# Kernel tuning notes

Measured on AMD Instinct MI355X. Metric: run time of the kernel, lower is better.

Reference implementation:

```python
import jax, jax.numpy as jnp
import numpy as np

HIDDEN = 128
N_RBF = 20
K = 16
CUTOFF = 5.0


def setup_inputs() -> dict:
    key = jax.random.key(0)
    ks = jax.random.split(key, 12)
    B, N, D = 8, 4096, HIDDEN
    edge_in = 2 * D + N_RBF  # 276
    s = 0.02
    return {
        "h": jax.random.normal(ks[0], (B, N, D), jnp.float32),
        "positions": jax.random.normal(ks[1], (B, N, 3), jnp.float32),
        # edge MLP: Linear(276->128), SiLU, Linear(128->128), SiLU
        "ew1": jax.random.normal(ks[2], (edge_in, D), jnp.float32) * s,
        "eb1": jnp.zeros((D,), jnp.float32),
        "ew2": jax.random.normal(ks[3], (D, D), jnp.float32) * s,
        "eb2": jnp.zeros((D,), jnp.float32),
        # node MLP: Linear(256->128), SiLU, (Dropout=identity in eval), Linear(128->128)
        "nw1": jax.random.normal(ks[4], (2 * D, D), jnp.float32) * s,
        "nb1": jnp.zeros((D,), jnp.float32),
        "nw2": jax.random.normal(ks[5], (D, D), jnp.float32) * s,
        "nb2": jnp.zeros((D,), jnp.float32),
        # LayerNorm
        "gamma": jnp.ones((D,), jnp.float32),
        "beta": jnp.zeros((D,), jnp.float32),
    }


def reference(h, positions, ew1, eb1, ew2, eb2, nw1, nb1, nw2, nb2, gamma, beta):
    B, N, D = h.shape
    k = min(K, N - 1)

    # ---- kNN graph build (dense pairwise, self masked with +inf) ----
    diff = positions[:, :, None, :] - positions[:, None, :, :]      # [B,N,N,3]
    dists = jnp.sqrt(jnp.sum(diff * diff, axis=-1) + 1e-8)          # [B,N,N]
    eye = jnp.eye(N, dtype=bool)
    dists_masked = jnp.where(eye[None], jnp.inf, dists)
    _, edge_idx = jax.lax.top_k(-dists_masked, k)                   # [B,N,k] smallest dists
    edge_dist = jnp.take_along_axis(dists_masked, edge_idx, axis=-1)  # [B,N,k]
    edge_mask = edge_dist < CUTOFF                                  # [B,N,k]

    # ---- RBF distance encoding (non-trainable buffers) ----
    centers = jnp.linspace(0.0, CUTOFF, N_RBF)                      # [n_rbf]
    widths = (CUTOFF / N_RBF) ** (-2)
    rbf = jnp.exp(-widths * (edge_dist[..., None] - centers) ** 2)  # [B,N,k,n_rbf]

    # ---- gather neighbor features ----
    h_j = jax.vmap(lambda hb, ib: hb[ib])(h, edge_idx)              # [B,N,k,D]
    h_i = jnp.broadcast_to(h[:, :, None, :], h_j.shape)             # [B,N,k,D]
    edge_features = jnp.concatenate([h_i, h_j, rbf], axis=-1)       # [B,N,k,2D+n_rbf]

    # ---- edge MLP + mask + scatter-sum aggregate ----
    m = jax.nn.silu(edge_features @ ew1 + eb1)
    m = jax.nn.silu(m @ ew2 + eb2)
    m = m * edge_mask[..., None].astype(m.dtype)
    agg = jnp.sum(m, axis=2)                                        # [B,N,D]

    # ---- node MLP (dropout is identity at eval) + residual + LayerNorm ----
    node_in = jnp.concatenate([h, agg], axis=-1)                    # [B,N,2D]
    update = jax.nn.silu(node_in @ nw1 + nb1) @ nw2 + nb2
    x = h + update
    mu = jnp.mean(x, axis=-1, keepdims=True)
    var = jnp.mean((x - mu) ** 2, axis=-1, keepdims=True)
    return (x - mu) / jnp.sqrt(var + 1e-5) * gamma + beta
```

## Files before the change

kernel.cpp:

```cpp
#include <hip/hip_runtime.h>
#include <hip/hip_bf16.h>

#define HID 128
#define NRBF 20
#define KNN 16
#define NNODE 4096
#define NBATCH 8

typedef __attribute__((ext_vector_type(8))) short short8;
typedef __attribute__((ext_vector_type(4))) float f32x4;

__device__ __forceinline__ short f2bf(float x) {
  __hip_bfloat16 b = __float2bfloat16(x);
  return __builtin_bit_cast(short, b);
}
__device__ __forceinline__ float silu_f(float x) {
  return x * __builtin_amdgcn_rcpf(1.0f + __expf(-x));
}
__device__ __forceinline__ short8 cv8(const float* p) {
  f32x4 a = *(const f32x4*)p;
  f32x4 b = *(const f32x4*)(p + 4);
  short8 r;
  r[0]=f2bf(a[0]); r[1]=f2bf(a[1]); r[2]=f2bf(a[2]); r[3]=f2bf(a[3]);
  r[4]=f2bf(b[0]); r[5]=f2bf(b[1]); r[6]=f2bf(b[2]); r[7]=f2bf(b[3]);
  return r;
}

__global__ __launch_bounds__(512)
void knn_kernel(const float* __restrict__ pos,
                int* __restrict__ eidx, float* __restrict__ edist)
{
  __shared__ f32x4 posL4[NNODE];
  __shared__ float d2b[8][128];
  __shared__ int   jb[8][128];
  __shared__ int   cntL[8];

  const int tid  = threadIdx.x;
  const int wv   = tid >> 6;
  const int lane = tid & 63;
  const int b    = blockIdx.x >> 7;
  const int grp  = blockIdx.x & 127;

  const float* pb = pos + (size_t)b * NNODE * 3;
  for (int idx = tid; idx < NNODE; idx += 512) {
    f32x4 v; v[0] = pb[idx*3]; v[1] = pb[idx*3+1]; v[2] = pb[idx*3+2]; v[3] = 0.f;
    posL4[idx] = v;
  }
  __syncthreads();

  const int i0 = grp * 32 + wv * 4;
  f32x4 pn[4];
  #pragma unroll
  for (int n = 0; n < 4; ++n) pn[n] = posL4[i0 + n];

  float vmin[4] = {3.0e38f, 3.0e38f, 3.0e38f, 3.0e38f};
  for (int t = 0; t < 64; ++t) {
    const int j = t * 64 + lane;
    f32x4 p = posL4[j];
    #pragma unroll
    for (int n = 0; n < 4; ++n) {
      float dx = __fsub_rn(pn[n][0], p[0]);
      float dy = __fsub_rn(pn[n][1], p[1]);
      float dz = __fsub_rn(pn[n][2], p[2]);
      float d2 = __fadd_rn(__fadd_rn(__fmul_rn(dx,dx), __fmul_rn(dy,dy)), __fmul_rn(dz,dz));
      if (j == i0 + n) d2 = 3.0e38f;
      vmin[n] = fminf(vmin[n], d2);
    }
  }

  float Ts[4];
  #pragma unroll
  for (int n = 0; n < 4; ++n) {
    float v = vmin[n];
    #pragma unroll
    for (int k = 2; k <= 64; k <<= 1) {
      #pragma unroll
      for (int jj = k >> 1; jj > 0; jj >>= 1) {
        float o = __shfl_xor(v, jj);
        const bool up   = ((lane & k) == 0);
        const bool lowl = ((lane & jj) == 0);
        float mn = fminf(v, o), mx = fmaxf(v, o);
        v = (up == lowl) ? mn : mx;
      }
    }
    Ts[n] = __shfl(v, 15);
  }

  #pragma unroll 1
  for (int n = 0; n < 4; ++n) {
    const int i = i0 + n;
    const float pix = pn[n][0], piy = pn[n][1], piz = pn[n][2];
    const float T = Ts[n];

    if (lane == 0) cntL[wv] = 0;
    for (int t = 0; t < 64; ++t) {
      const int j = t * 64 + lane;
      f32x4 p = posL4[j];
      float dx = __fsub_rn(pix, p[0]);
      float dy = __fsub_rn(piy, p[1]);
      float dz = __fsub_rn(piz, p[2]);
      float d2 = __fadd_rn(__fadd_rn(__fmul_rn(dx,dx), __fmul_rn(dy,dy)), __fmul_rn(dz,dz));
      bool ok = (j != i) && (d2 <= T);
      if (ok) {
        int p2 = atomicAdd(&cntL[wv], 1);
        if (p2 < 128) { d2b[wv][p2] = d2; jb[wv][p2] = j; }
      }
    }
    int cnt = cntL[wv];
    if (cnt > 128) cnt = 128;

    for (int s = lane; s < cnt; s += 64) {
      float dm = d2b[wv][s]; int jm = jb[wv][s];
      int rank = 0;
      for (int c = 0; c < cnt; ++c) {
        float dc = d2b[wv][c]; int jc = jb[wv][c];
        if (dc < dm || (dc == dm && jc < jm)) ++rank;
      }
      if (rank < KNN) {
        size_t base = ((size_t)b * NNODE + i) * KNN;
        eidx[base + rank]  = b * NNODE + jm;
        edist[base + rank] = sqrtf(__fadd_rn(dm, 1e-8f));
      }
    }
  }
}

#define ENPW 16

__global__ __launch_bounds__(512)
void edge_kernel(const float* __restrict__ h,
                 const int* __restrict__ eidx, const float* __restrict__ edist,
                 const float* __restrict__ ew1, const float* __restrict__ eb1,
                 const float* __restrict__ ew2, const float* __restrict__ eb2,
                 float* __restrict__ agg)
{
  __shared__ __attribute__((aligned(16))) short8 F1[9*8*64];
  __shared__ __attribute__((aligned(16))) short8 F2[4*8*64];
  __shared__ __attribute__((aligned(16))) short m1s[8][2048];

  const int tid = threadIdx.x;
  for (int f = tid; f < 9*8*64; f += 512) {
    int kc = f >> 9, rem = f & 511, nf = rem >> 6, ln = rem & 63;
    int kb = kc*32 + (ln >> 4)*8, col = nf*16 + (ln & 15);
    short8 v;
    #pragma unroll
    for (int e = 0; e < 8; ++e) {
      int k = kb + e;
      v[e] = (k < 276) ? f2bf(ew1[k*128 + col]) : (short)0;
    }
    F1[f] = v;
  }
  for (int f = tid; f < 4*8*64; f += 512) {
    int kc = f >> 9, rem = f & 511, nf = rem >> 6, ln = rem & 63;
    int kb = kc*32 + (ln >> 4)*8, col = nf*16 + (ln & 15);
    short8 v;
    #pragma unroll
    for (int e = 0; e < 8; ++e) v[e] = f2bf(ew2[(kb + e)*128 + col]);
    F2[f] = v;
  }
  __syncthreads();

  const int wv = tid >> 6, lane = tid & 63;
  const int lo = lane & 15, hi = lane >> 4;
  short* m1w = &m1s[wv][0];

  float b1v[8], b2v[8];
  #pragma unroll
  for (int nf = 0; nf < 8; ++nf) {
    b1v[nf] = eb1[nf*16 + lo];
    b2v[nf] = eb2[nf*16 + lo];
  }
  int wbase[4], xmask[4], rbase[4];
  #pragma unroll
  for (int q = 0; q < 4; ++q) {
    int row = hi*4 + q;
    wbase[q] = (row << 8) + (lo << 1);
    xmask[q] = (row & 7) << 4;
  }
  #pragma unroll
  for (int kc = 0; kc < 4; ++kc)
    rbase[kc] = ((lo << 8) + ((kc*32 + hi*8) << 1)) ^ ((lo & 7) << 4);

  const f32x4 zero4 = {0.f, 0.f, 0.f, 0.f};
  const int nbase = (blockIdx.x * 8 + wv) * ENPW;

  #pragma unroll 1
  for (int it = 0; it < ENPW/2; ++it) {
    const int nA = nbase + it*2, nB = nA + 1;
    int jgA = eidx[(size_t)nA*KNN + lo] & (NBATCH*NNODE - 1);
    int jgB = eidx[(size_t)nB*KNN + lo] & (NBATCH*NNODE - 1);
    const float deA = edist[(size_t)nA*KNN + lo];
    const float deB = edist[(size_t)nB*KNN + lo];

    short8 aIA[4], aJA[4], aIB[4], aJB[4];
    #pragma unroll
    for (int kc = 0; kc < 4; ++kc) {
      aIA[kc] = cv8(h + (size_t)nA*HID  + kc*32 + hi*8);
      aJA[kc] = cv8(h + (size_t)jgA*HID + kc*32 + hi*8);
      aIB[kc] = cv8(h + (size_t)nB*HID  + kc*32 + hi*8);
      aJB[kc] = cv8(h + (size_t)jgB*HID + kc*32 + hi*8);
    }
    short8 aRA, aRB;
    #pragma unroll
    for (int e = 0; e < 8; ++e) {
      const int r = hi*8 + e;
      float vA = 0.f, vB = 0.f;
      if (r < NRBF) {
        const float cr = (float)(r * (5.0/19.0));
        float tA = __fsub_rn(deA, cr), tB = __fsub_rn(deB, cr);
        vA = __expf(-16.0f * __fmul_rn(tA, tA));
        vB = __expf(-16.0f * __fmul_rn(tB, tB));
      }
      aRA[e] = f2bf(vA); aRB[e] = f2bf(vB);
    }

    f32x4 acc1A[8], acc1B[8];
    #pragma unroll
    for (int nf = 0; nf < 8; ++nf) { acc1A[nf] = zero4; acc1B[nf] = zero4; }
    #pragma unroll
    for (int kc = 0; kc < 9; ++kc) {
      short8 aA = (kc < 4) ? aIA[kc] : ((kc < 8) ? aJA[kc-4] : aRA);
      short8 aB = (kc < 4) ? aIB[kc] : ((kc < 8) ? aJB[kc-4] : aRB);
      #pragma unroll
      for (int nf = 0; nf < 8; ++nf) {
        short8 bf = F1[(kc*8 + nf)*64 + lane];
        acc1A[nf] = __builtin_amdgcn_mfma_f32_16x16x32_bf16(aA, bf, acc1A[nf], 0,0,0);
        acc1B[nf] = __builtin_amdgcn_mfma_f32_16x16x32_bf16(aB, bf, acc1B[nf], 0,0,0);
      }
    }

    short8 a2A[4], a2B[4];
    #pragma unroll
    for (int nf = 0; nf < 8; ++nf) {
      #pragma unroll
      for (int q = 0; q < 4; ++q) {
        int off = (wbase[q] + (nf << 5)) ^ xmask[q];
        *(short*)((char*)m1w + off) = f2bf(silu_f(acc1A[nf][q] + b1v[nf]));
      }
    }
    #pragma unroll
    for (int kc = 0; kc < 4; ++kc)
      a2A[kc] = *(const short8*)((char*)m1w + rbase[kc]);
    #pragma unroll
    for (int nf = 0; nf < 8; ++nf) {
      #pragma unroll
      for (int q = 0; q < 4; ++q) {
        int off = (wbase[q] + (nf << 5)) ^ xmask[q];
        *(short*)((char*)m1w + off) = f2bf(silu_f(acc1B[nf][q] + b1v[nf]));
      }
    }
    #pragma unroll
    for (int kc = 0; kc < 4; ++kc)
      a2B[kc] = *(const short8*)((char*)m1w + rbase[kc]);

    f32x4 acc2A[8], acc2B[8];
    #pragma unroll
    for (int nf = 0; nf < 8; ++nf) { acc2A[nf] = zero4; acc2B[nf] = zero4; }
    #pragma unroll
    for (int kc = 0; kc < 4; ++kc) {
      #pragma unroll
      for (int nf = 0; nf < 8; ++nf) {
        short8 bf = F2[(kc*8 + nf)*64 + lane];
        acc2A[nf] = __builtin_amdgcn_mfma_f32_16x16x32_bf16(a2A[kc], bf, acc2A[nf], 0,0,0);
        acc2B[nf] = __builtin_amdgcn_mfma_f32_16x16x32_bf16(a2B[kc], bf, acc2B[nf], 0,0,0);
      }
    }

    float dqA[4], dqB[4];
    #pragma unroll
    for (int q = 0; q < 4; ++q) {
      dqA[q] = edist[(size_t)nA*KNN + hi*4 + q];
      dqB[q] = edist[(size_t)nB*KNN + hi*4 + q];
    }
    #pragma unroll
    for (int nf = 0; nf < 8; ++nf) {
      float sA = 0.f, sB = 0.f;
      #pragma unroll
      for (int q = 0; q < 4; ++q) {
        float mA = silu_f(acc2A[nf][q] + b2v[nf]);
        float mB = silu_f(acc2B[nf][q] + b2v[nf]);
        sA += (dqA[q] < 5.0f) ? mA : 0.f;
        sB += (dqB[q] < 5.0f) ? mB : 0.f;
      }
      sA += __shfl_xor(sA, 16); sA += __shfl_xor(sA, 32);
      sB += __shfl_xor(sB, 16); sB += __shfl_xor(sB, 32);
      if (hi == 0) {
        agg[(size_t)nA*HID + nf*16 + lo] = sA;
        agg[(size_t)nB*HID + nf*16 + lo] = sB;
      }
    }
  }
}

__global__ __launch_bounds__(512)
void node_kernel(const float* __restrict__ h, const float* agg,
                 const float* __restrict__ nw1, const float* __restrict__ nb1,
                 const float* __restrict__ nw2, const float* __restrict__ nb2,
                 const float* __restrict__ gam, const float* __restrict__ bet,
                 float* out)
{
  __shared__ __attribute__((aligned(16))) short8 G1[8*8*64];
  __shared__ __attribute__((aligned(16))) short8 G2[4*8*64];
  __shared__ __attribute__((aligned(16))) short m1s[8][2048];

  const int tid = threadIdx.x;
  for (int f = tid; f < 8*8*64; f += 512) {
    int kc = f >> 9, rem = f & 511, nf = rem >> 6, ln = rem & 63;
    int kb = kc*32 + (ln >> 4)*8, col = nf*16 + (ln & 15);
    short8 v;
    #pragma unroll
    for (int e = 0; e < 8; ++e) v[e] = f2bf(nw1[(kb + e)*128 + col]);
    G1[f] = v;
  }
  for (int f = tid; f < 4*8*64; f += 512) {
    int kc = f >> 9, rem = f & 511, nf = rem >> 6, ln = rem & 63;
    int kb = kc*32 + (ln >> 4)*8, col = nf*16 + (ln & 15);
    short8 v;
    #pragma unroll
    for (int e = 0; e < 8; ++e) v[e] = f2bf(nw2[(kb + e)*128 + col]);
    G2[f] = v;
  }
  __syncthreads();

  const int wv = tid >> 6, lane = tid & 63;
  const int lo = lane & 15, hi = lane >> 4;
  short* m1w = &m1s[wv][0];

  float b1v[8], b2v[8], gv[8], bv[8];
  #pragma unroll
  for (int nf = 0; nf < 8; ++nf) {
    b1v[nf] = nb1[nf*16 + lo];
    b2v[nf] = nb2[nf*16 + lo];
    gv[nf]  = gam[nf*16 + lo];
    bv[nf]  = bet[nf*16 + lo];
  }
  const f32x4 zero4 = {0.f, 0.f, 0.f, 0.f};

  const int row0 = (blockIdx.x * 8 + wv) * 16;

  const float* hrow = h   + (size_t)(row0 + lo) * HID;
  const float* arow = agg + (size_t)(row0 + lo) * HID;

  f32x4 acc1[8];
  #pragma unroll
  for (int nf = 0; nf < 8; ++nf) acc1[nf] = zero4;
  #pragma unroll
  for (int kc = 0; kc < 8; ++kc) {
    short8 a = (kc < 4) ? cv8(hrow + kc*32 + hi*8)
                        : cv8(arow + (kc - 4)*32 + hi*8);
    #pragma unroll
    for (int nf = 0; nf < 8; ++nf) {
      short8 bf = G1[(kc*8 + nf)*64 + lane];
      acc1[nf] = __builtin_amdgcn_mfma_f32_16x16x32_bf16(a, bf, acc1[nf], 0,0,0);
    }
  }

  #pragma unroll
  for (int nf = 0; nf < 8; ++nf) {
    #pragma unroll
    for (int q = 0; q < 4; ++q) {
      float s = silu_f(acc1[nf][q] + b1v[nf]);
      int row = hi*4 + q, col = nf*16 + lo;
      int byteoff = ((row << 8) + (col << 1)) ^ ((row & 7) << 4);
      *(short*)((char*)m1w + byteoff) = f2bf(s);
    }
  }

  f32x4 acc2[8];
  #pragma unroll
  for (int nf = 0; nf < 8; ++nf) acc2[nf] = zero4;
  #pragma unroll
  for (int kc = 0; kc < 4; ++kc) {
    int byteA = ((lo << 8) + ((kc*32 + hi*8) << 1)) ^ ((lo & 7) << 4);
    short8 a = *(const short8*)((char*)m1w + byteA);
    #pragma unroll
    for (int nf = 0; nf < 8; ++nf) {
      short8 bf = G2[(kc*8 + nf)*64 + lane];
      acc2[nf] = __builtin_amdgcn_mfma_f32_16x16x32_bf16(a, bf, acc2[nf], 0,0,0);
    }
  }

  float xv[4][8];
  #pragma unroll
  for (int nf = 0; nf < 8; ++nf) {
    #pragma unroll
    for (int q = 0; q < 4; ++q) {
      xv[q][nf] = acc2[nf][q] + b2v[nf]
                + h[(size_t)(row0 + hi*4 + q) * HID + nf*16 + lo];
    }
  }

  #pragma unroll
  for (int q = 0; q < 4; ++q) {
    float s = 0.0f;
    #pragma unroll
    for (int nf = 0; nf < 8; ++nf) s += xv[q][nf];
    s += __shfl_xor(s, 1); s += __shfl_xor(s, 2);
    s += __shfl_xor(s, 4); s += __shfl_xor(s, 8);
    float mu = s * 0.0078125f;
    float t = 0.0f;
    #pragma unroll
    for (int nf = 0; nf < 8; ++nf) { float d = xv[q][nf] - mu; t += d * d; }
    t += __shfl_xor(t, 1); t += __shfl_xor(t, 2);
    t += __shfl_xor(t, 4); t += __shfl_xor(t, 8);
    float inv = 1.0f / sqrtf(t * 0.0078125f + 1e-5f);
    #pragma unroll
    for (int nf = 0; nf < 8; ++nf) {
      float y = (xv[q][nf] - mu) * inv * gv[nf] + bv[nf];
      out[(size_t)(row0 + hi*4 + q) * HID + nf*16 + lo] = y;
    }
  }
}

extern "C" void kernel_launch(void* const* d_in, const int* in_sizes, int n_in,
                              void* d_out, int out_size, void* d_ws, size_t ws_size,
                              hipStream_t stream) {
  (void)in_sizes; (void)n_in; (void)out_size;
  const float* h   = (const float*)d_in[0];
  const float* pos = (const float*)d_in[1];
  const float* ew1 = (const float*)d_in[2];
  const float* eb1 = (const float*)d_in[3];
  const float* ew2 = (const float*)d_in[4];
  const float* eb2 = (const float*)d_in[5];
  const float* nw1 = (const float*)d_in[6];
  const float* nb1 = (const float*)d_in[7];
  const float* nw2 = (const float*)d_in[8];
  const float* nb2 = (const float*)d_in[9];
  const float* gam = (const float*)d_in[10];
  const float* bet = (const float*)d_in[11];

  const size_t need = (size_t)NBATCH * NNODE * KNN * 8;
  if (ws_size < need) return;

  char* wsp = (char*)d_ws;
  int*   eidx  = (int*)wsp;
  float* edist = (float*)(wsp + (size_t)NBATCH * NNODE * KNN * 4);
  float* agg   = (float*)d_out;

  knn_kernel<<<dim3(1024), dim3(512), 0, stream>>>(pos, eidx, edist);
  edge_kernel<<<dim3(256), dim3(512), 0, stream>>>(h, eidx, edist, ew1, eb1, ew2, eb2, agg);
  node_kernel<<<dim3(256), dim3(512), 0, stream>>>(h, agg, nw1, nb1, nw2, nb2, gam, bet,
                                                   (float*)d_out);
}
```

Before: 237.3 us.

## Pre-convert h to bf16, batch kNN candidate collection, and raise MFMA priority

```diff
diff --git a/kernel.cpp b/kernel.cpp
--- a/kernel.cpp
+++ b/kernel.cpp
@@ -1,18 +1,19 @@
 #include <hip/hip_runtime.h>
-#include <hip/hip_bf16.h>
 
 #define HID 128
 #define NRBF 20
 #define KNN 16
 #define NNODE 4096
 #define NBATCH 8
+#define CAP 112
 
 typedef __attribute__((ext_vector_type(8))) short short8;
 typedef __attribute__((ext_vector_type(4))) float f32x4;
 
 __device__ __forceinline__ short f2bf(float x) {
-  __hip_bfloat16 b = __float2bfloat16(x);
-  return __builtin_bit_cast(short, b);
+  unsigned u = __builtin_bit_cast(unsigned, x);
+  u = u + 0x7FFFu + ((u >> 16) & 1u);
+  return (short)(u >> 16);
 }
 __device__ __forceinline__ float silu_f(float x) {
   return x * __builtin_amdgcn_rcpf(1.0f + __expf(-x));
@@ -26,14 +27,21 @@
   return r;
 }
 
+__global__ __launch_bounds__(256)
+void hcvt_kernel(const float* __restrict__ h, short* __restrict__ hb)
+{
+  size_t i = ((size_t)blockIdx.x * 256 + threadIdx.x) * 8;
+  *(short8*)(hb + i) = cv8(h + i);
+}
+
 __global__ __launch_bounds__(512)
 void knn_kernel(const float* __restrict__ pos,
                 int* __restrict__ eidx, float* __restrict__ edist)
 {
-  __shared__ f32x4 posL4[NNODE];
-  __shared__ float d2b[8][128];
-  __shared__ int   jb[8][128];
-  __shared__ int   cntL[8];
+  __shared__ float pX[NNODE], pY[NNODE], pZ[NNODE];
+  __shared__ float d2b[8][4][CAP];
+  __shared__ int   jb[8][4][CAP];
+  __shared__ int   cntL[8][4];
 
   const int tid  = threadIdx.x;
   const int wv   = tid >> 6;
@@ -43,27 +51,26 @@
 
   const float* pb = pos + (size_t)b * NNODE * 3;
   for (int idx = tid; idx < NNODE; idx += 512) {
-    f32x4 v; v[0] = pb[idx*3]; v[1] = pb[idx*3+1]; v[2] = pb[idx*3+2]; v[3] = 0.f;
-    posL4[idx] = v;
+    pX[idx] = pb[idx*3]; pY[idx] = pb[idx*3+1]; pZ[idx] = pb[idx*3+2];
   }
   __syncthreads();
 
   const int i0 = grp * 32 + wv * 4;
-  f32x4 pn[4];
-  #pragma unroll
-  for (int n = 0; n < 4; ++n) pn[n] = posL4[i0 + n];
+  float pix[4], piy[4], piz[4];
+  #pragma unroll
+  for (int n = 0; n < 4; ++n) { pix[n]=pX[i0+n]; piy[n]=pY[i0+n]; piz[n]=pZ[i0+n]; }
 
   float vmin[4] = {3.0e38f, 3.0e38f, 3.0e38f, 3.0e38f};
+  #pragma unroll 4
   for (int t = 0; t < 64; ++t) {
     const int j = t * 64 + lane;
-    f32x4 p = posL4[j];
+    const float x = pX[j], y = pY[j], z = pZ[j];
     #pragma unroll
     for (int n = 0; n < 4; ++n) {
-      float dx = __fsub_rn(pn[n][0], p[0]);
-      float dy = __fsub_rn(pn[n][1], p[1]);
-      float dz = __fsub_rn(pn[n][2], p[2]);
+      float dx = __fsub_rn(pix[n], x);
+      float dy = __fsub_rn(piy[n], y);
+      float dz = __fsub_rn(piz[n], z);
       float d2 = __fadd_rn(__fadd_rn(__fmul_rn(dx,dx), __fmul_rn(dy,dy)), __fmul_rn(dz,dz));
-      if (j == i0 + n) d2 = 3.0e38f;
       vmin[n] = fminf(vmin[n], d2);
     }
   }
@@ -83,41 +90,40 @@
         v = (up == lowl) ? mn : mx;
       }
     }
-    Ts[n] = __shfl(v, 15);
+    Ts[n] = __shfl(v, 16);
+  }
+
+  if (lane < 4) cntL[wv][lane] = 0;
+  #pragma unroll 2
+  for (int t = 0; t < 64; ++t) {
+    const int j = t * 64 + lane;
+    const float x = pX[j], y = pY[j], z = pZ[j];
+    #pragma unroll
+    for (int n = 0; n < 4; ++n) {
+      float dx = __fsub_rn(pix[n], x);
+      float dy = __fsub_rn(piy[n], y);
+      float dz = __fsub_rn(piz[n], z);
+      float d2 = __fadd_rn(__fadd_rn(__fmul_rn(dx,dx), __fmul_rn(dy,dy)), __fmul_rn(dz,dz));
+      if ((j != i0 + n) && (d2 <= Ts[n])) {
+        int p = atomicAdd(&cntL[wv][n], 1);
+        if (p < CAP) { d2b[wv][n][p] = d2; jb[wv][n][p] = j; }
+      }
+    }
   }
 
   #pragma unroll 1
   for (int n = 0; n < 4; ++n) {
-    const int i = i0 + n;
-    const float pix = pn[n][0], piy = pn[n][1], piz = pn[n][2];
-    const float T = Ts[n];
-
-    if (lane == 0) cntL[wv] = 0;
-    for (int t = 0; t < 64; ++t) {
-      const int j = t * 64 + lane;
-      f32x4 p = posL4[j];
-      float dx = __fsub_rn(pix, p[0]);
-      float dy = __fsub_rn(piy, p[1]);
-      float dz = __fsub_rn(piz, p[2]);
-      float d2 = __fadd_rn(__fadd_rn(__fmul_rn(dx,dx), __fmul_rn(dy,dy)), __fmul_rn(dz,dz));
-      bool ok = (j != i) && (d2 <= T);
-      if (ok) {
-        int p2 = atomicAdd(&cntL[wv], 1);
-        if (p2 < 128) { d2b[wv][p2] = d2; jb[wv][p2] = j; }
-      }
-    }
-    int cnt = cntL[wv];
-    if (cnt > 128) cnt = 128;
-
+    int cnt = cntL[wv][n];
+    if (cnt > CAP) cnt = CAP;
     for (int s = lane; s < cnt; s += 64) {
-      float dm = d2b[wv][s]; int jm = jb[wv][s];
+      float dm = d2b[wv][n][s]; int jm = jb[wv][n][s];
       int rank = 0;
       for (int c = 0; c < cnt; ++c) {
-        float dc = d2b[wv][c]; int jc = jb[wv][c];
+        float dc = d2b[wv][n][c]; int jc = jb[wv][n][c];
         if (dc < dm || (dc == dm && jc < jm)) ++rank;
       }
       if (rank < KNN) {
-        size_t base = ((size_t)b * NNODE + i) * KNN;
+        size_t base = ((size_t)b * NNODE + i0 + n) * KNN;
         eidx[base + rank]  = b * NNODE + jm;
         edist[base + rank] = sqrtf(__fadd_rn(dm, 1e-8f));
       }
@@ -127,8 +133,9 @@
 
 #define ENPW 16
 
+template<bool HBF>
 __global__ __launch_bounds__(512)
-void edge_kernel(const float* __restrict__ h,
+void edge_kernel(const float* __restrict__ h, const short* __restrict__ hb,
                  const int* __restrict__ eidx, const float* __restrict__ edist,
                  const float* __restrict__ ew1, const float* __restrict__ eb1,
                  const float* __restrict__ ew2, const float* __restrict__ eb2,
@@ -195,10 +202,17 @@
     short8 aIA[4], aJA[4], aIB[4], aJB[4];
     #pragma unroll
     for (int kc = 0; kc < 4; ++kc) {
-      aIA[kc] = cv8(h + (size_t)nA*HID  + kc*32 + hi*8);
-      aJA[kc] = cv8(h + (size_t)jgA*HID + kc*32 + hi*8);
-      aIB[kc] = cv8(h + (size_t)nB*HID  + kc*32 + hi*8);
-      aJB[kc] = cv8(h + (size_t)jgB*HID + kc*32 + hi*8);
+      if constexpr (HBF) {
+        aIA[kc] = *(const short8*)(hb + (size_t)nA*HID  + kc*32 + hi*8);
+        aJA[kc] = *(const short8*)(hb + (size_t)jgA*HID + kc*32 + hi*8);
+        aIB[kc] = *(const short8*)(hb + (size_t)nB*HID  + kc*32 + hi*8);
+        aJB[kc] = *(const short8*)(hb + (size_t)jgB*HID + kc*32 + hi*8);
+      } else {
+        aIA[kc] = cv8(h + (size_t)nA*HID  + kc*32 + hi*8);
+        aJA[kc] = cv8(h + (size_t)jgA*HID + kc*32 + hi*8);
+        aIB[kc] = cv8(h + (size_t)nB*HID  + kc*32 + hi*8);
+        aJB[kc] = cv8(h + (size_t)jgB*HID + kc*32 + hi*8);
+      }
     }
     short8 aRA, aRB;
     #pragma unroll
@@ -217,6 +231,7 @@
     f32x4 acc1A[8], acc1B[8];
     #pragma unroll
     for (int nf = 0; nf < 8; ++nf) { acc1A[nf] = zero4; acc1B[nf] = zero4; }
+    __builtin_amdgcn_s_setprio(1);
     #pragma unroll
     for (int kc = 0; kc < 9; ++kc) {
       short8 aA = (kc < 4) ? aIA[kc] : ((kc < 8) ? aJA[kc-4] : aRA);
@@ -228,6 +243,7 @@
         acc1B[nf] = __builtin_amdgcn_mfma_f32_16x16x32_bf16(aB, bf, acc1B[nf], 0,0,0);
       }
     }
+    __builtin_amdgcn_s_setprio(0);
 
     short8 a2A[4], a2B[4];
     #pragma unroll
@@ -256,6 +272,7 @@
     f32x4 acc2A[8], acc2B[8];
     #pragma unroll
     for (int nf = 0; nf < 8; ++nf) { acc2A[nf] = zero4; acc2B[nf] = zero4; }
+    __builtin_amdgcn_s_setprio(1);
     #pragma unroll
     for (int kc = 0; kc < 4; ++kc) {
       #pragma unroll
@@ -265,6 +282,7 @@
         acc2B[nf] = __builtin_amdgcn_mfma_f32_16x16x32_bf16(a2B[kc], bf, acc2B[nf], 0,0,0);
       }
     }
+    __builtin_amdgcn_s_setprio(0);
 
     float dqA[4], dqB[4];
     #pragma unroll
@@ -292,8 +310,10 @@
   }
 }
 
+template<bool HBF>
 __global__ __launch_bounds__(512)
-void node_kernel(const float* __restrict__ h, const float* agg,
+void node_kernel(const float* __restrict__ h, const short* __restrict__ hb,
+                 const float* agg,
                  const float* __restrict__ nw1, const float* __restrict__ nb1,
                  const float* __restrict__ nw2, const float* __restrict__ nb2,
                  const float* __restrict__ gam, const float* __restrict__ bet,
@@ -340,14 +360,20 @@
 
   const float* hrow = h   + (size_t)(row0 + lo) * HID;
   const float* arow = agg + (size_t)(row0 + lo) * HID;
+  const short* hbrow = hb + (size_t)(row0 + lo) * HID;
 
   f32x4 acc1[8];
   #pragma unroll
   for (int nf = 0; nf < 8; ++nf) acc1[nf] = zero4;
   #pragma unroll
   for (int kc = 0; kc < 8; ++kc) {
-    short8 a = (kc < 4) ? cv8(hrow + kc*32 + hi*8)
-                        : cv8(arow + (kc - 4)*32 + hi*8);
+    short8 a;
+    if (kc < 4) {
+      if constexpr (HBF) a = *(const short8*)(hbrow + kc*32 + hi*8);
+      else               a = cv8(hrow + kc*32 + hi*8);
+    } else {
+      a = cv8(arow + (kc - 4)*32 + hi*8);
+    }
     #pragma unroll
     for (int nf = 0; nf < 8; ++nf) {
       short8 bf = G1[(kc*8 + nf)*64 + lane];
@@ -429,16 +455,30 @@
   const float* gam = (const float*)d_in[10];
   const float* bet = (const float*)d_in[11];
 
-  const size_t need = (size_t)NBATCH * NNODE * KNN * 8;
-  if (ws_size < need) return;
+  const size_t base_need = (size_t)NBATCH * NNODE * KNN * 8;
+  const size_t hbf_need  = base_need + (size_t)NBATCH * NNODE * HID * 2;
+  if (ws_size < base_need) return;
+  const bool use_hbf = (ws_size >= hbf_need);
 
   char* wsp = (char*)d_ws;
   int*   eidx  = (int*)wsp;
   float* edist = (float*)(wsp + (size_t)NBATCH * NNODE * KNN * 4);
+  short* hb    = (short*)(wsp + base_need);
   float* agg   = (float*)d_out;
 
+  if (use_hbf) {
+    hcvt_kernel<<<dim3(2048), dim3(256), 0, stream>>>(h, hb);
+  }
   knn_kernel<<<dim3(1024), dim3(512), 0, stream>>>(pos, eidx, edist);
-  edge_kernel<<<dim3(256), dim3(512), 0, stream>>>(h, eidx, edist, ew1, eb1, ew2, eb2, agg);
-  node_kernel<<<dim3(256), dim3(512), 0, stream>>>(h, agg, nw1, nb1, nw2, nb2, gam, bet,
-                                                   (float*)d_out);
-}
+  if (use_hbf) {
+    edge_kernel<true ><<<dim3(256), dim3(512), 0, stream>>>(h, hb, eidx, edist,
+                                                            ew1, eb1, ew2, eb2, agg);
+    node_kernel<true ><<<dim3(256), dim3(512), 0, stream>>>(h, hb, agg, nw1, nb1,
+                                                            nw2, nb2, gam, bet, (float*)d_out);
+  } else {
+    edge_kernel<false><<<dim3(256), dim3(512), 0, stream>>>(h, hb, eidx, edist,
+                                                            ew1, eb1, ew2, eb2, agg);
+    node_kernel<false><<<dim3(256), dim3(512), 0, stream>>>(h, hb, agg, nw1, nb1,
+                                                            nw2, nb2, gam, bet, (float*)d_out);
+  }
+}
```

After: 211.7 us. -10.8%, faster.
